# Kernel optimization log

Measured on AMD Instinct MI355X. Metric: run time of the kernel, lower is better.

## Reference

```python
import jax, jax.numpy as jnp
import numpy as np

D_IN = 4096
NUM_HEADS = 32
NUM_KV_GROUPS = 8
HEAD_DIM = D_IN // NUM_HEADS  # 128 (init overwrites head_dim)
GROUP_SIZE = NUM_HEADS // NUM_KV_GROUPS
SEQ = 2048
BATCH = 1
EPS = 1e-6


def layernorm(t, w, b):
    mu = jnp.mean(t, axis=-1, keepdims=True)
    var = jnp.var(t, axis=-1, keepdims=True)
    return (t - mu) * jax.lax.rsqrt(var + EPS) * w + b


def rope(t, cos, sin):
    # t: [B, H, S, D]; cos/sin: [S, D] broadcast over B, H
    half = t.shape[-1] // 2
    x1, x2 = t[..., :half], t[..., half:]
    rot = jnp.concatenate([-x2, x1], axis=-1)
    return t * cos + rot * sin


def setup_inputs() -> dict:
    key = jax.random.key(0)
    ks = jax.random.split(key, 10)
    x = jax.random.normal(ks[0], (BATCH, SEQ, D_IN), dtype=jnp.float32)
    mask = jnp.triu(jnp.ones((SEQ, SEQ), dtype=bool), k=1)  # True = masked (causal)
    # RoPE tables
    inv_freq = 1.0 / (10000.0 ** (np.arange(0, HEAD_DIM, 2, dtype=np.float32) / HEAD_DIM))
    pos = np.arange(SEQ, dtype=np.float32)
    ang = np.einsum('s,d->sd', pos, inv_freq)  # [S, D/2]
    ang = np.concatenate([ang, ang], axis=-1)  # [S, D]
    cos = jnp.asarray(np.cos(ang))
    sin = jnp.asarray(np.sin(ang))
    s = 0.02
    Wq = jax.random.normal(ks[1], (D_IN, NUM_HEADS * HEAD_DIM), dtype=jnp.float32) * s
    Wk = jax.random.normal(ks[2], (D_IN, NUM_KV_GROUPS * HEAD_DIM), dtype=jnp.float32) * s
    Wv = jax.random.normal(ks[3], (D_IN, NUM_KV_GROUPS * HEAD_DIM), dtype=jnp.float32) * s
    Wo = jax.random.normal(ks[4], (NUM_HEADS * HEAD_DIM, D_IN), dtype=jnp.float32) * s
    qn_w = jnp.ones((HEAD_DIM,), jnp.float32)
    qn_b = jnp.zeros((HEAD_DIM,), jnp.float32)
    kn_w = jnp.ones((HEAD_DIM,), jnp.float32)
    kn_b = jnp.zeros((HEAD_DIM,), jnp.float32)
    return {"x": x, "mask": mask, "cos": cos, "sin": sin, "Wq": Wq, "Wk": Wk,
            "Wv": Wv, "Wo": Wo, "qn_w": qn_w, "qn_b": qn_b, "kn_w": kn_w, "kn_b": kn_b}


def reference(x, mask, cos, sin, Wq, Wk, Wv, Wo, qn_w, qn_b, kn_w, kn_b):
    B, S, _ = x.shape
    q = (x @ Wq).reshape(B, S, NUM_HEADS, HEAD_DIM).transpose(0, 2, 1, 3)      # [B,H,S,D]
    k = (x @ Wk).reshape(B, S, NUM_KV_GROUPS, HEAD_DIM).transpose(0, 2, 1, 3)  # [B,G,S,D]
    v = (x @ Wv).reshape(B, S, NUM_KV_GROUPS, HEAD_DIM).transpose(0, 2, 1, 3)
    q = layernorm(q, qn_w, qn_b)
    k = layernorm(k, kn_w, kn_b)
    q = rope(q, cos, sin)
    k = rope(k, cos, sin)
    k = jnp.repeat(k, GROUP_SIZE, axis=1)  # [B,H,S,D]
    v = jnp.repeat(v, GROUP_SIZE, axis=1)
    scores = jnp.einsum('bhqd,bhkd->bhqk', q, k)
    scores = jnp.where(mask, -jnp.inf, scores)
    attn = jax.nn.softmax(scores / jnp.sqrt(jnp.float32(HEAD_DIM)), axis=-1)
    ctx = jnp.einsum('bhqk,bhkd->bhqd', attn, v)
    ctx = ctx.transpose(0, 2, 1, 3).reshape(B, S, NUM_HEADS * HEAD_DIM)
    return ctx @ Wo
```

## Files before the change

### kernel.cpp

```cpp
#include <hip/hip_runtime.h>
#include <stdint.h>

#define SQ   2048
#define DIN  4096
#define NH   32
#define NKV  8
#define HD   128
#define NQKV 6144

typedef float f32x4 __attribute__((ext_vector_type(4)));
typedef short bf16x8 __attribute__((ext_vector_type(8)));

__device__ __forceinline__ short f2bf(float f) {
  union { float f; uint32_t u; } v; v.f = f;
  uint32_t r = (v.u + 0x7FFFu + ((v.u >> 16) & 1u)) >> 16;
  return (short)r;
}

__device__ __forceinline__ void gl2lds(const void* g, void* l) {
  __builtin_amdgcn_global_load_lds(
      (const __attribute__((address_space(1))) void*)g,
      (__attribute__((address_space(3))) void*)l, 16, 0, 0);
}

__global__ void cvt_bf16(const float* __restrict__ src, short* __restrict__ dst, long n) {
  long i = ((long)blockIdx.x * blockDim.x + threadIdx.x) * 4;
  if (i + 3 < n) {
    float4 v = *(const float4*)(src + i);
    short o[4] = { f2bf(v.x), f2bf(v.y), f2bf(v.z), f2bf(v.w) };
    *(uint2*)(dst + i) = *(uint2*)o;
  }
}

__global__ __launch_bounds__(256) void transpose_cvt(const float* __restrict__ src, int ldS, long zS,
                                                     short* __restrict__ dst, int ldD, long zD) {
  __shared__ float tile[64][65];
  src += (long)blockIdx.z * zS;
  dst += (long)blockIdx.z * zD;
  int r0 = blockIdx.y * 64, c0 = blockIdx.x * 64;
  int tid = threadIdx.x;
#pragma unroll
  for (int i = 0; i < 16; ++i) {
    int idx = i * 256 + tid;
    int rr = idx >> 6, cc = idx & 63;
    tile[rr][cc] = src[(long)(r0 + rr) * ldS + c0 + cc];
  }
  __syncthreads();
#pragma unroll
  for (int i = 0; i < 16; ++i) {
    int idx = i * 256 + tid;
    int dr = idx >> 6, dc = idx & 63;
    dst[(long)(c0 + dr) * ldD + r0 + dc] = f2bf(tile[dc][dr]);
  }
}

#define BM 128
#define BN 128
#define BK 32
__global__ __launch_bounds__(256) void gemm_bf16(const short* __restrict__ A, const short* __restrict__ Bt,
                                                 float* __restrict__ C, int M, int N, int K) {
  __shared__ __align__(16) short As[BM * BK];
  __shared__ __align__(16) short Bs[BN * BK];
  int tid = threadIdx.x;
  int wave = tid >> 6, lane = tid & 63;
  int l16 = lane & 15, lq = lane >> 4;
  int m0 = blockIdx.y * BM, n0 = blockIdx.x * BN;
  int wm = (wave >> 1) * 64, wn = (wave & 1) * 64;
  int ch = (lane & 3) ^ ((lane >> 3) & 3);
  f32x4 acc[4][4] = {};
  for (int k0 = 0; k0 < K; k0 += BK) {
#pragma unroll
    for (int c = 0; c < 2; ++c) {
      int call = wave * 2 + c;
      int r = call * 16 + (lane >> 2);
      gl2lds(&A[(long)(m0 + r) * K + k0 + ch * 8], &As[call * 512]);
      gl2lds(&Bt[(long)(n0 + r) * K + k0 + ch * 8], &Bs[call * 512]);
    }
    __syncthreads();
    bf16x8 af[4], bfr[4];
#pragma unroll
    for (int i = 0; i < 4; ++i) {
      int row = wm + i * 16 + l16;
      af[i] = *(const bf16x8*)&As[row * BK + (lq ^ ((row >> 1) & 3)) * 8];
    }
#pragma unroll
    for (int j = 0; j < 4; ++j) {
      int row = wn + j * 16 + l16;
      bfr[j] = *(const bf16x8*)&Bs[row * BK + (lq ^ ((row >> 1) & 3)) * 8];
    }
#pragma unroll
    for (int i = 0; i < 4; ++i)
#pragma unroll
      for (int j = 0; j < 4; ++j)
        acc[i][j] = __builtin_amdgcn_mfma_f32_16x16x32_bf16(af[i], bfr[j], acc[i][j], 0, 0, 0);
    __syncthreads();
  }
#pragma unroll
  for (int i = 0; i < 4; ++i)
#pragma unroll
    for (int j = 0; j < 4; ++j)
#pragma unroll
      for (int r = 0; r < 4; ++r) {
        int row = m0 + wm + i * 16 + lq * 4 + r;
        int col = n0 + wn + j * 16 + l16;
        C[(long)row * N + col] = acc[i][j][r];
      }
}

__global__ __launch_bounds__(64) void ln_rope(const float* __restrict__ qkv,
                                              const float* __restrict__ cosb, const float* __restrict__ sinb,
                                              const float* __restrict__ qw, const float* __restrict__ qb,
                                              const float* __restrict__ kw, const float* __restrict__ kb,
                                              short* __restrict__ qo, short* __restrict__ ko) {
  int s = blockIdx.x, slice = blockIdx.y, t = threadIdx.x;
  bool isq = slice < NH;
  int off = isq ? slice * HD : DIN + (slice - NH) * HD;
  const float* src = qkv + (long)s * NQKV + off;
  float v0 = src[t], v1 = src[t + 64];
  float sum = v0 + v1, ss = v0 * v0 + v1 * v1;
#pragma unroll
  for (int o = 1; o < 64; o <<= 1) { sum += __shfl_xor(sum, o); ss += __shfl_xor(ss, o); }
  float mu = sum * (1.f / 128.f);
  float var = ss * (1.f / 128.f) - mu * mu;
  float rstd = rsqrtf(var + 1e-6f);
  const float* w  = isq ? qw : kw;
  const float* bb = isq ? qb : kb;
  float n0 = (v0 - mu) * rstd * w[t]      + bb[t];
  float n1 = (v1 - mu) * rstd * w[t + 64] + bb[t + 64];
  float c0 = cosb[s * HD + t], c1 = cosb[s * HD + t + 64];
  float s0 = sinb[s * HD + t], s1 = sinb[s * HD + t + 64];
  float o0 = n0 * c0 - n1 * s0;
  float o1 = n1 * c1 + n0 * s1;
  short* dst = isq ? (qo + ((long)slice * SQ + s) * HD)
                   : (ko + ((long)(slice - NH) * SQ + s) * HD);
  dst[t] = f2bf(o0);
  dst[t + 64] = f2bf(o1);
}

__global__ __launch_bounds__(256) void attn(const short* __restrict__ q, const short* __restrict__ k,
                                            const short* __restrict__ vT, short* __restrict__ ctx) {
  int pair = blockIdx.x, h = blockIdx.y, g = h >> 2;
  int tid = threadIdx.x, w = tid >> 6, lane = tid & 63;
  int l16 = lane & 15, lq = lane >> 4;
  __shared__ __align__(16) short Ks[64 * 128];
  __shared__ __align__(16) short Vs[128 * 64];
  __shared__ __align__(16) short pbuf[4][16 * 72];
  const short* qh = q + (long)h * SQ * HD;
  const short* kg = k + (long)g * SQ * HD;
  const short* vg = vT + (long)g * HD * SQ;
  int kr = (w * 4) * 4 + (lane >> 4);
  int vrw = (w * 4) * 8 + (lane >> 3);
  const float sc = 0.08838834764831845f * 1.4426950408889634f;

  for (int st = 0; st < 2; ++st) {
    int qt = st ? (31 - pair) : pair;
    int qbase = qt * 64 + w * 16;
    bf16x8 aq[4];
#pragma unroll
    for (int kk = 0; kk < 4; ++kk)
      aq[kk] = *(const bf16x8*)&qh[(long)(qbase + l16) * HD + kk * 32 + lq * 8];
    float m_r[4], l_r[4];
    f32x4 acc[8] = {};
#pragma unroll
    for (int r = 0; r < 4; ++r) { m_r[r] = -__builtin_inff(); l_r[r] = 0.f; }

    for (int kt = 0; kt <= qt; ++kt) {
#pragma unroll
      for (int j = 0; j < 4; ++j) {
        int call = w * 4 + j;
        int r = kr + j * 4;
        int chk = (lane & 15) ^ (r & 15);
        gl2lds(&kg[(long)(kt * 64 + r) * HD + chk * 8], &Ks[call * 512]);
        int rv = vrw + j * 8;
        int chv = (lane & 7) ^ (rv & 7);
        gl2lds(&vg[(long)rv * SQ + kt * 64 + chv * 8], &Vs[call * 512]);
      }
      __syncthreads();
      f32x4 s4[4];
#pragma unroll
      for (int b = 0; b < 4; ++b) s4[b] = (f32x4){0.f, 0.f, 0.f, 0.f};
#pragma unroll
      for (int b = 0; b < 4; ++b) {
        int krow = b * 16 + l16;
#pragma unroll
        for (int kk = 0; kk < 4; ++kk) {
          bf16x8 bk = *(const bf16x8*)&Ks[krow * 128 + ((kk * 4 + lq) ^ (krow & 15)) * 8];
          s4[b] = __builtin_amdgcn_mfma_f32_16x16x32_bf16(aq[kk], bk, s4[b], 0, 0, 0);
        }
      }
      int qrow0 = qbase + lq * 4;
#pragma unroll
      for (int b = 0; b < 4; ++b) {
        int key = kt * 64 + b * 16 + l16;
#pragma unroll
        for (int r = 0; r < 4; ++r) {
          float val = s4[b][r] * sc;
          s4[b][r] = (key > qrow0 + r) ? -__builtin_inff() : val;
        }
      }
      float p[4][4];
#pragma unroll
      for (int r = 0; r < 4; ++r) {
        float mx = fmaxf(fmaxf(s4[0][r], s4[1][r]), fmaxf(s4[2][r], s4[3][r]));
#pragma unroll
        for (int o = 1; o < 16; o <<= 1) mx = fmaxf(mx, __shfl_xor(mx, o));
        float mnew = fmaxf(m_r[r], mx);
        float alpha = exp2f(m_r[r] - mnew);
        float sum = 0.f;
#pragma unroll
        for (int b = 0; b < 4; ++b) { float pv = exp2f(s4[b][r] - mnew); p[b][r] = pv; sum += pv; }
#pragma unroll
        for (int o = 1; o < 16; o <<= 1) sum += __shfl_xor(sum, o);
        l_r[r] = l_r[r] * alpha + sum;
        m_r[r] = mnew;
#pragma unroll
        for (int n = 0; n < 8; ++n) acc[n][r] *= alpha;
      }
#pragma unroll
      for (int b = 0; b < 4; ++b)
#pragma unroll
        for (int r = 0; r < 4; ++r)
          pbuf[w][(lq * 4 + r) * 72 + b * 16 + l16] = f2bf(p[b][r]);
#pragma unroll
      for (int kk = 0; kk < 2; ++kk) {
        bf16x8 pf = *(const bf16x8*)&pbuf[w][l16 * 72 + kk * 32 + lq * 8];
#pragma unroll
        for (int n = 0; n < 8; ++n) {
          int vrow = n * 16 + l16;
          bf16x8 vf = *(const bf16x8*)&Vs[vrow * 64 + ((kk * 4 + lq) ^ (vrow & 7)) * 8];
          acc[n] = __builtin_amdgcn_mfma_f32_16x16x32_bf16(pf, vf, acc[n], 0, 0, 0);
        }
      }
      __syncthreads();
    }
#pragma unroll
    for (int n = 0; n < 8; ++n)
#pragma unroll
      for (int r = 0; r < 4; ++r) {
        int srow = qbase + lq * 4 + r;
        ctx[(long)srow * (NH * HD) + h * HD + n * 16 + l16] = f2bf(acc[n][r] / l_r[r]);
      }
  }
}

#define XB_OFF     0L
#define QR_OFF     0L
#define WQKVT_OFF  16777216L
#define KR_OFF     16777216L
#define VT_OFF     20971520L
#define CTX_OFF    25165824L
#define WOT_OFF    67108864L
#define QKV_OFF    100663296L

extern "C" void kernel_launch(void* const* d_in, const int* in_sizes, int n_in,
                              void* d_out, int out_size, void* d_ws, size_t ws_size,
                              hipStream_t stream) {
  const float* x    = (const float*)d_in[0];
  const float* cosb = (const float*)d_in[2];
  const float* sinb = (const float*)d_in[3];
  const float* Wq   = (const float*)d_in[4];
  const float* Wk   = (const float*)d_in[5];
  const float* Wv   = (const float*)d_in[6];
  const float* Wo   = (const float*)d_in[7];
  const float* qnw  = (const float*)d_in[8];
  const float* qnb  = (const float*)d_in[9];
  const float* knw  = (const float*)d_in[10];
  const float* knb  = (const float*)d_in[11];

  char* ws = (char*)d_ws;
  short* xb    = (short*)(ws + XB_OFF);
  short* qr    = (short*)(ws + QR_OFF);
  short* wqkvt = (short*)(ws + WQKVT_OFF);
  short* krp   = (short*)(ws + KR_OFF);
  short* vt    = (short*)(ws + VT_OFF);
  short* ctx   = (short*)(ws + CTX_OFF);
  short* wot   = (short*)(ws + WOT_OFF);
  float* qkv   = (float*)(ws + QKV_OFF);

  cvt_bf16<<<8192, 256, 0, stream>>>(x, xb, (long)SQ * DIN);
  transpose_cvt<<<dim3(64, 64, 1), 256, 0, stream>>>(Wq, 4096, 0L, wqkvt, 4096, 0L);
  transpose_cvt<<<dim3(16, 64, 1), 256, 0, stream>>>(Wk, 1024, 0L, wqkvt + (long)4096 * 4096, 4096, 0L);
  transpose_cvt<<<dim3(16, 64, 1), 256, 0, stream>>>(Wv, 1024, 0L, wqkvt + (long)5120 * 4096, 4096, 0L);
  transpose_cvt<<<dim3(64, 64, 1), 256, 0, stream>>>(Wo, 4096, 0L, wot, 4096, 0L);
  gemm_bf16<<<dim3(NQKV / BN, SQ / BM), 256, 0, stream>>>(xb, wqkvt, qkv, SQ, NQKV, DIN);
  ln_rope<<<dim3(SQ, NH + NKV), 64, 0, stream>>>(qkv, cosb, sinb, qnw, qnb, knw, knb, qr, krp);
  transpose_cvt<<<dim3(2, 32, 8), 256, 0, stream>>>(qkv + 5120, NQKV, 128L, vt, SQ, (long)HD * SQ);
  attn<<<dim3(16, NH), 256, 0, stream>>>(qr, krp, vt, ctx);
  gemm_bf16<<<dim3(DIN / BN, SQ / BM), 256, 0, stream>>>(ctx, wot, (float*)d_out, SQ, DIN, DIN);
}
```

Baseline: 611.3 us.

## Replace GEMM with 8-wave triple-buffered pipelined kernel with XCD-aware tile remap

Replaces the simple 128x128x32 bf16 GEMM with a 512-thread kernel computing 128x256 tiles at BK=64. It uses three LDS buffers so global-to-LDS loads for step t+2 overlap MFMA work on step t, interleaving load issue with four MFMA phases under s_setprio. It also remaps block indices so consecutive tiles spread across the 8 XCDs, which should improve L2 reuse. The goal is to hide memory latency and cut barrier overhead in the QKV and output projections, at the cost of fragile hand-placed waitcnt and barrier scheduling and higher LDS use.

```diff
diff --git a/kernel.cpp b/kernel.cpp
--- a/kernel.cpp
+++ b/kernel.cpp
@@ -54,57 +54,123 @@
   }
 }
 
-#define BM 128
-#define BN 128
-#define BK 32
-__global__ __launch_bounds__(256) void gemm_bf16(const short* __restrict__ A, const short* __restrict__ Bt,
+#define TSZ 24576
+#define MFMA(d, a, b) d = __builtin_amdgcn_mfma_f32_16x16x32_bf16(a, b, d, 0, 0, 0)
+
+__global__ __launch_bounds__(512, 2) void gemm8p(const short* __restrict__ A, const short* __restrict__ Bt,
                                                  float* __restrict__ C, int M, int N, int K) {
-  __shared__ __align__(16) short As[BM * BK];
-  __shared__ __align__(16) short Bs[BN * BK];
+  __shared__ __align__(16) short lds[3 * TSZ];
+  int nwg = gridDim.x;
+  int lin = ((int)blockIdx.x & 7) * (nwg >> 3) + ((int)blockIdx.x >> 3);
+  int mt = M >> 7;
+  int m0 = (lin % mt) * 128, n0 = (lin / mt) * 256;
+
   int tid = threadIdx.x;
-  int wave = tid >> 6, lane = tid & 63;
+  int w = tid >> 6, lane = tid & 63;
   int l16 = lane & 15, lq = lane >> 4;
-  int m0 = blockIdx.y * BM, n0 = blockIdx.x * BN;
-  int wm = (wave >> 1) * 64, wn = (wave & 1) * 64;
-  int ch = (lane & 3) ^ ((lane >> 3) & 3);
+  int wm = (w >> 2) * 64, wn = (w & 3) * 64;
+  int sx = l16 & 7;
+  int fo0 = ((lq ^ sx) << 3) + (l16 << 6);
+  int fo1 = (((lq + 4) ^ sx) << 3) + (l16 << 6);
+
+  int srow = lane >> 3;
+  int g8 = (lane & 7) ^ srow;
+  long a8K = 8L * K;
+  const short* aS = A + (long)(m0 + w * 16 + srow) * K + g8 * 8;
+  const short* bS = Bt + (long)(n0 + w * 32 + srow) * K + g8 * 8;
+
   f32x4 acc[4][4] = {};
-  for (int k0 = 0; k0 < K; k0 += BK) {
-#pragma unroll
-    for (int c = 0; c < 2; ++c) {
-      int call = wave * 2 + c;
-      int r = call * 16 + (lane >> 2);
-      gl2lds(&A[(long)(m0 + r) * K + k0 + ch * 8], &As[call * 512]);
-      gl2lds(&Bt[(long)(n0 + r) * K + k0 + ch * 8], &Bs[call * 512]);
+  const int KT = K >> 6;
+
+#pragma unroll
+  for (int tt = 0; tt < 2; ++tt) {
+    short* base = lds + tt * TSZ;
+    gl2lds(aS + tt * 64, base + (w * 2) * 512);
+    gl2lds(aS + a8K + tt * 64, base + (w * 2 + 1) * 512);
+#pragma unroll
+    for (int j = 0; j < 4; ++j)
+      gl2lds(bS + j * a8K + tt * 64, base + 8192 + (w * 4 + j) * 512);
+  }
+  asm volatile("s_waitcnt vmcnt(6)" ::: "memory");
+  __builtin_amdgcn_s_barrier();
+
+  for (int t = 0; t < KT; ++t) {
+    const short* wA = lds + (t % 3) * TSZ + wm * 64;
+    const short* wB = lds + (t % 3) * TSZ + 8192 + wn * 64;
+    int sb = (t + 2) % 3;
+    short* stA = lds + sb * TSZ + (w * 2) * 512;
+    short* stB = lds + sb * TSZ + 8192 + (w * 4) * 512;
+    long ko = (long)(t + 2) * 64;
+    bool doStage = (t + 2 < KT);
+
+    bf16x8 aAk0, aAk1, aBk0, aBk1, bAk0, bAk1, bBk0, bBk1;
+
+    aAk0 = *(const bf16x8*)(wA + fo0);        aAk1 = *(const bf16x8*)(wA + fo1);
+    aBk0 = *(const bf16x8*)(wA + 1024 + fo0); aBk1 = *(const bf16x8*)(wA + 1024 + fo1);
+    bAk0 = *(const bf16x8*)(wB + fo0);        bAk1 = *(const bf16x8*)(wB + fo1);
+    bBk0 = *(const bf16x8*)(wB + 1024 + fo0); bBk1 = *(const bf16x8*)(wB + 1024 + fo1);
+    if (doStage) { gl2lds(bS + ko, stB); gl2lds(bS + a8K + ko, stB + 512); }
+    __builtin_amdgcn_s_barrier();
+    asm volatile("s_waitcnt lgkmcnt(0)" ::: "memory");
+    __builtin_amdgcn_s_setprio(1);
+    MFMA(acc[0][0], aAk0, bAk0); MFMA(acc[0][1], aAk0, bBk0);
+    MFMA(acc[1][0], aBk0, bAk0); MFMA(acc[1][1], aBk0, bBk0);
+    MFMA(acc[0][0], aAk1, bAk1); MFMA(acc[0][1], aAk1, bBk1);
+    MFMA(acc[1][0], aBk1, bAk1); MFMA(acc[1][1], aBk1, bBk1);
+    __builtin_amdgcn_s_setprio(0);
+    __builtin_amdgcn_s_barrier();
+
+    bAk0 = *(const bf16x8*)(wB + 2048 + fo0); bAk1 = *(const bf16x8*)(wB + 2048 + fo1);
+    bBk0 = *(const bf16x8*)(wB + 3072 + fo0); bBk1 = *(const bf16x8*)(wB + 3072 + fo1);
+    if (doStage) { gl2lds(bS + 2 * a8K + ko, stB + 1024); gl2lds(bS + 3 * a8K + ko, stB + 1536); }
+    __builtin_amdgcn_s_barrier();
+    asm volatile("s_waitcnt lgkmcnt(0)" ::: "memory");
+    __builtin_amdgcn_s_setprio(1);
+    MFMA(acc[0][2], aAk0, bAk0); MFMA(acc[0][3], aAk0, bBk0);
+    MFMA(acc[1][2], aBk0, bAk0); MFMA(acc[1][3], aBk0, bBk0);
+    MFMA(acc[0][2], aAk1, bAk1); MFMA(acc[0][3], aAk1, bBk1);
+    MFMA(acc[1][2], aBk1, bAk1); MFMA(acc[1][3], aBk1, bBk1);
+    __builtin_amdgcn_s_setprio(0);
+    __builtin_amdgcn_s_barrier();
+
+    aAk0 = *(const bf16x8*)(wA + 2048 + fo0); aAk1 = *(const bf16x8*)(wA + 2048 + fo1);
+    aBk0 = *(const bf16x8*)(wA + 3072 + fo0); aBk1 = *(const bf16x8*)(wA + 3072 + fo1);
+    if (doStage) { gl2lds(aS + ko, stA); }
+    __builtin_amdgcn_s_barrier();
+    asm volatile("s_waitcnt lgkmcnt(0)" ::: "memory");
+    __builtin_amdgcn_s_setprio(1);
+    MFMA(acc[2][2], aAk0, bAk0); MFMA(acc[2][3], aAk0, bBk0);
+    MFMA(acc[3][2], aBk0, bAk0); MFMA(acc[3][3], aBk0, bBk0);
+    MFMA(acc[2][2], aAk1, bAk1); MFMA(acc[2][3], aAk1, bBk1);
+    MFMA(acc[3][2], aBk1, bAk1); MFMA(acc[3][3], aBk1, bBk1);
+    __builtin_amdgcn_s_setprio(0);
+    __builtin_amdgcn_s_barrier();
+
+    bAk0 = *(const bf16x8*)(wB + fo0);        bAk1 = *(const bf16x8*)(wB + fo1);
+    bBk0 = *(const bf16x8*)(wB + 1024 + fo0); bBk1 = *(const bf16x8*)(wB + 1024 + fo1);
+    if (doStage) { gl2lds(aS + a8K + ko, stA + 512); }
+    __builtin_amdgcn_s_barrier();
+    asm volatile("s_waitcnt lgkmcnt(0)" ::: "memory");
+    __builtin_amdgcn_s_setprio(1);
+    MFMA(acc[2][0], aAk0, bAk0); MFMA(acc[2][1], aAk0, bBk0);
+    MFMA(acc[3][0], aBk0, bAk0); MFMA(acc[3][1], aBk0, bBk0);
+    MFMA(acc[2][0], aAk1, bAk1); MFMA(acc[2][1], aAk1, bBk1);
+    MFMA(acc[3][0], aBk1, bAk1); MFMA(acc[3][1], aBk1, bBk1);
+    __builtin_amdgcn_s_setprio(0);
+    if (t < KT - 1) {
+      if (doStage) asm volatile("s_waitcnt vmcnt(6)" ::: "memory");
+      else         asm volatile("s_waitcnt vmcnt(0)" ::: "memory");
+      __builtin_amdgcn_s_barrier();
     }
-    __syncthreads();
-    bf16x8 af[4], bfr[4];
-#pragma unroll
-    for (int i = 0; i < 4; ++i) {
-      int row = wm + i * 16 + l16;
-      af[i] = *(const bf16x8*)&As[row * BK + (lq ^ ((row >> 1) & 3)) * 8];
-    }
-#pragma unroll
-    for (int j = 0; j < 4; ++j) {
-      int row = wn + j * 16 + l16;
-      bfr[j] = *(const bf16x8*)&Bs[row * BK + (lq ^ ((row >> 1) & 3)) * 8];
-    }
-#pragma unroll
-    for (int i = 0; i < 4; ++i)
-#pragma unroll
-      for (int j = 0; j < 4; ++j)
-        acc[i][j] = __builtin_amdgcn_mfma_f32_16x16x32_bf16(af[i], bfr[j], acc[i][j], 0, 0, 0);
-    __syncthreads();
-  }
+  }
+
 #pragma unroll
   for (int i = 0; i < 4; ++i)
 #pragma unroll
     for (int j = 0; j < 4; ++j)
 #pragma unroll
-      for (int r = 0; r < 4; ++r) {
-        int row = m0 + wm + i * 16 + lq * 4 + r;
-        int col = n0 + wn + j * 16 + l16;
-        C[(long)row * N + col] = acc[i][j][r];
-      }
+      for (int r = 0; r < 4; ++r)
+        C[(long)(m0 + wm + i * 16 + lq * 4 + r) * N + n0 + wn + j * 16 + l16] = acc[i][j][r];
 }
 
 __global__ __launch_bounds__(64) void ln_rope(const float* __restrict__ qkv,
@@ -282,9 +348,9 @@
   transpose_cvt<<<dim3(16, 64, 1), 256, 0, stream>>>(Wk, 1024, 0L, wqkvt + (long)4096 * 4096, 4096, 0L);
   transpose_cvt<<<dim3(16, 64, 1), 256, 0, stream>>>(Wv, 1024, 0L, wqkvt + (long)5120 * 4096, 4096, 0L);
   transpose_cvt<<<dim3(64, 64, 1), 256, 0, stream>>>(Wo, 4096, 0L, wot, 4096, 0L);
-  gemm_bf16<<<dim3(NQKV / BN, SQ / BM), 256, 0, stream>>>(xb, wqkvt, qkv, SQ, NQKV, DIN);
+  gemm8p<<<(SQ / 128) * (NQKV / 256), 512, 0, stream>>>(xb, wqkvt, qkv, SQ, NQKV, DIN);
   ln_rope<<<dim3(SQ, NH + NKV), 64, 0, stream>>>(qkv, cosb, sinb, qnw, qnb, knw, knb, qr, krp);
   transpose_cvt<<<dim3(2, 32, 8), 256, 0, stream>>>(qkv + 5120, NQKV, 128L, vt, SQ, (long)HD * SQ);
   attn<<<dim3(16, NH), 256, 0, stream>>>(qr, krp, vt, ctx);
-  gemm_bf16<<<dim3(DIN / BN, SQ / BM), 256, 0, stream>>>(ctx, wot, (float*)d_out, SQ, DIN, DIN);
-}
+  gemm8p<<<(SQ / 128) * (DIN / 256), 512, 0, stream>>>(ctx, wot, (float*)d_out, SQ, DIN, DIN);
+}
```

Result: faster. 584.1 us (-4.4%).
